# Optimization experiments

Measured on AMD Instinct MI355X. Metric: run time of the kernel, lower is better.

## Reference

```python
import jax, jax.numpy as jnp
import numpy as np

N, T, IN_DIM = 5000, 100, 32
FEAT, HID, OUT, HEADS = 64, 64, 8, 4
E = 160000
F_IN = FEAT + OUT  # GATCell input = concat(embedding, theta)


def setup_inputs() -> dict:
    key = jax.random.key(0)
    ks = jax.random.split(key, 16)
    s = 0.05
    d = {}
    d["x"] = jax.random.normal(ks[0], (N, T, IN_DIM), jnp.float32)
    d["edge_index"] = jax.random.randint(ks[1], (2, E), 0, N, dtype=jnp.int32)
    # LSTM params (PyTorch gate order: i, f, g, o)
    d["W_ih"] = jax.random.normal(ks[2], (IN_DIM, 4 * FEAT), jnp.float32) * s
    d["W_hh"] = jax.random.normal(ks[3], (FEAT, 4 * FEAT), jnp.float32) * s
    d["b_ih"] = jax.random.normal(ks[4], (4 * FEAT,), jnp.float32) * s
    d["b_hh"] = jax.random.normal(ks[5], (4 * FEAT,), jnp.float32) * s
    # TransformerConv params (lin_q/k/v with bias, lin_skip with bias; concat=False)
    d["Wq"] = jax.random.normal(ks[6], (F_IN, HEADS * HID), jnp.float32) * s
    d["bq"] = jax.random.normal(ks[7], (HEADS * HID,), jnp.float32) * s
    d["Wk"] = jax.random.normal(ks[8], (F_IN, HEADS * HID), jnp.float32) * s
    d["bk"] = jax.random.normal(ks[9], (HEADS * HID,), jnp.float32) * s
    d["Wv"] = jax.random.normal(ks[10], (F_IN, HEADS * HID), jnp.float32) * s
    d["bv"] = jax.random.normal(ks[11], (HEADS * HID,), jnp.float32) * s
    d["Wskip"] = jax.random.normal(ks[12], (F_IN, HID), jnp.float32) * s
    d["bskip"] = jax.random.normal(ks[13], (HID,), jnp.float32) * s
    # GATCell mlp (bias=False)
    d["Wmlp"] = jax.random.normal(ks[14], (HID, OUT), jnp.float32) * s
    return d


def _lstm(x, W_ih, W_hh, b_ih, b_hh):
    # x: [N, T, IN_DIM] -> embedding [T, N, FEAT]
    xs = jnp.transpose(x, (1, 0, 2))

    def step(carry, xt):
        h, c = carry
        gates = xt @ W_ih + h @ W_hh + (b_ih + b_hh)
        i, f, g, o = jnp.split(gates, 4, axis=-1)
        c = jax.nn.sigmoid(f) * c + jax.nn.sigmoid(i) * jnp.tanh(g)
        h = jax.nn.sigmoid(o) * jnp.tanh(c)
        return (h, c), h

    h0 = jnp.zeros((x.shape[0], FEAT), x.dtype)
    _, hs = jax.lax.scan(step, (h0, h0), xs)
    return hs


def _transformer_conv(h, edge_index, Wq, bq, Wk, bk, Wv, bv, Wskip, bskip):
    # h: [N, F_IN]; edge_index: [2, E] (row 0 = source j, row 1 = target i)
    n = h.shape[0]
    src, dst = edge_index[0], edge_index[1]
    q = (h @ Wq + bq).reshape(n, HEADS, HID)
    k = (h @ Wk + bk).reshape(n, HEADS, HID)
    v = (h @ Wv + bv).reshape(n, HEADS, HID)
    # per-edge attention logits [E, HEADS]
    alpha = jnp.einsum('ehd,ehd->eh', q[dst], k[src]) / jnp.sqrt(jnp.float32(HID))
    # segment softmax over incoming edges of each target node
    m = jax.ops.segment_max(alpha, dst, num_segments=n)
    m = jnp.where(jnp.isfinite(m), m, 0.0)
    ex = jnp.exp(alpha - m[dst])
    denom = jax.ops.segment_sum(ex, dst, num_segments=n)
    w = ex / jnp.maximum(denom[dst], 1e-16)
    agg = jax.ops.segment_sum(w[:, :, None] * v[src], dst, num_segments=n)  # [N,H,D]
    out = agg.mean(axis=1)  # concat=False -> average heads
    return out + h @ Wskip + bskip  # root skip connection


def reference(x, edge_index, W_ih, W_hh, b_ih, b_hh, Wq, bq, Wk, bk, Wv, bv,
              Wskip, bskip, Wmlp):
    emb = _lstm(x, W_ih, W_hh, b_ih, b_hh)  # [T, N, FEAT]
    n = x.shape[0]

    def gat_step(theta, emb_t):
        h_in = jnp.concatenate([emb_t, theta], axis=-1)  # [N, F_IN]
        hid = _transformer_conv(h_in, edge_index, Wq, bq, Wk, bk, Wv, bv,
                                Wskip, bskip)
        theta_new = jnp.tanh(hid) @ Wmlp
        return theta_new, theta_new

    theta0 = jnp.zeros((n, OUT), x.dtype)
    _, thetas = jax.lax.scan(gat_step, theta0, emb)  # [T, N, OUT]
    theta = jnp.transpose(thetas, (1, 0, 2))  # [N, T, OUT]

    alpha_beta = theta[:, :, :-3]
    a_b = jax.nn.sigmoid(theta[:, :, -3:-1])
    a = a_b[:, :, 0:1] * a_b[:, :, 1:]
    b = a_b[:, :, 0:1] - a
    c = jax.nn.softplus(theta[:, :, -1:])
    return jnp.concatenate([alpha_beta, a, b, c], axis=-1)
```

## Files before the change

### kernel.cpp

```cpp
#include <hip/hip_runtime.h>
#include <math.h>

#define NN 5000
#define TT 100
#define IND 32
#define FEATD 64
#define HIDD 64
#define OUTD 8
#define NHEADS 4
#define EE 160000
#define FIN 72
#define NHC 256
#define ATTN_B 2500
#define LSTM_B 625

typedef float floatx2 __attribute__((ext_vector_type(2)));

__device__ __forceinline__ float fsig(float x){ return 1.f/(1.f+__expf(-x)); }
__device__ __forceinline__ float ftanh(float x){ return 1.f - 2.f/(__expf(2.f*x)+1.f); }
__device__ __forceinline__ float fsoftplus(float x){ return (x>20.f)? x : log1pf(__expf(x)); }

__global__ __launch_bounds__(256) void count_edges(const int* __restrict__ dst,
                                                   int* __restrict__ cnt){
    int e = blockIdx.x*256 + threadIdx.x;
    if (e < EE) atomicAdd(&cnt[dst[e]], 1);
}

#define SCAN_N 5120
__global__ __launch_bounds__(1024) void scan_csr(const int* __restrict__ cnt,
                                                 int* __restrict__ row_ptr,
                                                 int* __restrict__ cursor){
    __shared__ int sa[SCAN_N];
    __shared__ int sb[SCAN_N];
    int tid = threadIdx.x;
    for (int i=tid;i<SCAN_N;i+=1024) sa[i] = (i<NN)?cnt[i]:0;
    __syncthreads();
    int *s=sa, *d=sb;
    for (int off=1; off<SCAN_N; off<<=1){
        for (int i=tid;i<SCAN_N;i+=1024){
            int v = s[i];
            if (i>=off) v += s[i-off];
            d[i] = v;
        }
        __syncthreads();
        int* t=s; s=d; d=t;
    }
    for (int i=tid;i<=NN;i+=1024){
        int excl = (i==0)?0:s[i-1];
        row_ptr[i] = excl;
        if (i<NN) cursor[i] = excl;
    }
}

__global__ __launch_bounds__(256) void fill_edges(const int* __restrict__ src,
                                                  const int* __restrict__ dst,
                                                  int* __restrict__ cursor,
                                                  int* __restrict__ col){
    int e = blockIdx.x*256 + threadIdx.x;
    if (e < EE){
        int dn = dst[e];
        int pos = atomicAdd(&cursor[dn], 1);
        col[pos] = src[e];
    }
}

#define LOADKV(e) (*reinterpret_cast<const uint2*>(kv + (size_t)col[(e)]*512 + lane*8))
__global__ __launch_bounds__(256) void lstm_attn_step(
    const float* __restrict__ x,
    const float* __restrict__ W_ih, const float* __restrict__ W_hh,
    const float* __restrict__ b_ih, const float* __restrict__ b_hh,
    float* __restrict__ h, float* __restrict__ c,
    const float* __restrict__ q,
    const unsigned char* __restrict__ kv,
    const float* __restrict__ sk,
    const int* __restrict__ row_ptr,
    const int* __restrict__ col,
    const float* __restrict__ Wmlp,
    float* __restrict__ theta,
    float* __restrict__ out,
    int t)
{
    __shared__ float mrg[2][5][64];
    __shared__ float xh[8][96];
    int tid = threadIdx.x;

    if (blockIdx.x < ATTN_B){
        if (t == 0) return;
        int wvid = tid >> 6;
        int lane = tid & 63;
        int ln   = wvid >> 1;
        int half = wvid & 1;
        int n = blockIdx.x*2 + ln;
        int e0 = row_ptr[n], e1 = row_ptr[n+1];
        float4 qv = *reinterpret_cast<const float4*>(q + n*NHC + lane*4);
        qv.x *= 0.125f; qv.y *= 0.125f; qv.z *= 0.125f; qv.w *= 0.125f;

        float denA=0.f, denB=0.f;
        float aA0=0.f, aA1=0.f, aA2=0.f, aA3=0.f;
        float aB0=0.f, aB1=0.f, aB2=0.f, aB3=0.f;

        const uint2 zv = {0u,0u};
        uint2 bA0=zv, bA1=zv, bB0=zv, bB1=zv;
        int base = e0 + half;
        if (base     < e1) bA0 = LOADKV(base);
        if (base + 2 < e1) bB0 = LOADKV(base+2);
        if (base + 4 < e1) bA1 = LOADKV(base+4);
        if (base + 6 < e1) bB1 = LOADKV(base+6);
        for (int e = base; e < e1; e += 4){
            uint2 uA = bA0; bA0 = bA1; bA1 = zv;
            uint2 uB = bB0; bB0 = bB1; bB1 = zv;
            if (e + 8  < e1) bA1 = LOADKV(e+8);
            if (e + 10 < e1) bB1 = LOADKV(e+10);

            floatx2 kA0 = __builtin_amdgcn_cvt_pk_f32_fp8(uA.x, false);
            floatx2 kA1 = __builtin_amdgcn_cvt_pk_f32_fp8(uA.x, true);
            floatx2 kB0 = __builtin_amdgcn_cvt_pk_f32_fp8(uB.x, false);
            floatx2 kB1 = __builtin_amdgcn_cvt_pk_f32_fp8(uB.x, true);
            float pA = qv.x*kA0[0] + qv.y*kA0[1] + qv.z*kA1[0] + qv.w*kA1[1];
            float pB = qv.x*kB0[0] + qv.y*kB0[1] + qv.z*kB1[0] + qv.w*kB1[1];
            pA += __shfl_xor(pA,1); pB += __shfl_xor(pB,1);
            pA += __shfl_xor(pA,2); pB += __shfl_xor(pB,2);
            pA += __shfl_xor(pA,4); pB += __shfl_xor(pB,4);
            pA += __shfl_xor(pA,8); pB += __shfl_xor(pB,8);

            float eA = __expf(pA);
            float eB = __expf((e + 2 < e1) ? pB : -INFINITY);
            floatx2 vA0 = __builtin_amdgcn_cvt_pk_f32_fp8(uA.y, false);
            floatx2 vA1 = __builtin_amdgcn_cvt_pk_f32_fp8(uA.y, true);
            floatx2 vB0 = __builtin_amdgcn_cvt_pk_f32_fp8(uB.y, false);
            floatx2 vB1 = __builtin_amdgcn_cvt_pk_f32_fp8(uB.y, true);
            denA += eA;
            aA0 = fmaf(eA, vA0[0], aA0);
            aA1 = fmaf(eA, vA0[1], aA1);
            aA2 = fmaf(eA, vA1[0], aA2);
            aA3 = fmaf(eA, vA1[1], aA3);
            denB += eB;
            aB0 = fmaf(eB, vB0[0], aB0);
            aB1 = fmaf(eB, vB0[1], aB1);
            aB2 = fmaf(eB, vB1[0], aB2);
            aB3 = fmaf(eB, vB1[1], aB3);
        }
        float denom = denA + denB;
        float ax = aA0 + aB0;
        float ay = aA1 + aB1;
        float az = aA2 + aB2;
        float aw = aA3 + aB3;

        if (half == 1){
            mrg[ln][0][lane]=denom;
            mrg[ln][1][lane]=ax; mrg[ln][2][lane]=ay;
            mrg[ln][3][lane]=az; mrg[ln][4][lane]=aw;
        }
        __syncthreads();
        if (half == 1) return;

        denom += mrg[ln][0][lane];
        ax += mrg[ln][1][lane];
        ay += mrg[ln][2][lane];
        az += mrg[ln][3][lane];
        aw += mrg[ln][4][lane];

        float inv = 1.f / fmaxf(denom, 1e-16f);
        ax *= inv; ay *= inv; az *= inv; aw *= inv;
        ax += __shfl_xor(ax,16); ax += __shfl_xor(ax,32);
        ay += __shfl_xor(ay,16); ay += __shfl_xor(ay,32);
        az += __shfl_xor(az,16); az += __shfl_xor(az,32);
        aw += __shfl_xor(aw,16); aw += __shfl_xor(aw,32);
        int d0 = (lane & 15) * 4;
        float4 skv = *reinterpret_cast<const float4*>(sk + n*64 + d0);
        float t0 = ftanh(0.25f*ax + skv.x);
        float t1 = ftanh(0.25f*ay + skv.y);
        float t2 = ftanh(0.25f*az + skv.z);
        float t3 = ftanh(0.25f*aw + skv.w);
        float p8[8];
        #pragma unroll
        for (int j=0;j<8;j++){
            p8[j] = fmaf(t0, Wmlp[(d0+0)*8+j],
                    fmaf(t1, Wmlp[(d0+1)*8+j],
                    fmaf(t2, Wmlp[(d0+2)*8+j],
                         t3* Wmlp[(d0+3)*8+j])));
        }
        #pragma unroll
        for (int j=0;j<8;j++){
            p8[j] += __shfl_xor(p8[j],1);
            p8[j] += __shfl_xor(p8[j],2);
            p8[j] += __shfl_xor(p8[j],4);
            p8[j] += __shfl_xor(p8[j],8);
        }
        if (lane == 0){
            float4 t0v = {p8[0],p8[1],p8[2],p8[3]};
            float4 t1v = {p8[4],p8[5],p8[6],p8[7]};
            *reinterpret_cast<float4*>(theta + n*8)     = t0v;
            *reinterpret_cast<float4*>(theta + n*8 + 4) = t1v;
            float ab0 = fsig(p8[5]);
            float ab1 = fsig(p8[6]);
            float a  = ab0*ab1;
            float bb = ab0 - a;
            float cc = fsoftplus(p8[7]);
            float4 o0 = {p8[0],p8[1],p8[2],p8[3]};
            float4 o1 = {p8[4],a,bb,cc};
            float* op = out + ((size_t)n*TT + (t-1))*8;
            *reinterpret_cast<float4*>(op)     = o0;
            *reinterpret_cast<float4*>(op + 4) = o1;
        }
    } else {
        if (t >= TT) return;
        int n0 = (blockIdx.x - ATTN_B) * 8;
        for (int i=tid; i<8*96; i+=256){
            int node = i/96, kk = i%96;
            int n = n0 + node;
            xh[node][kk] = (kk<32) ? x[(n*TT + t)*IND + kk] : h[n*64 + (kk-32)];
        }
        __syncthreads();

        int d  = tid & 63;
        int wv = tid >> 6;
        float acc[2][4];
        #pragma unroll
        for (int p=0;p<2;p++){
            #pragma unroll
            for (int g=0;g<4;g++) acc[p][g]=0.f;
        }
        #pragma unroll 8
        for (int kk=0; kk<32; kk++){
            const float* Wr = W_ih + kk*256;
            float w0=Wr[d], w1=Wr[d+64], w2=Wr[d+128], w3=Wr[d+192];
            float x0 = xh[wv][kk], x1 = xh[wv+4][kk];
            acc[0][0]=fmaf(x0,w0,acc[0][0]); acc[0][1]=fmaf(x0,w1,acc[0][1]);
            acc[0][2]=fmaf(x0,w2,acc[0][2]); acc[0][3]=fmaf(x0,w3,acc[0][3]);
            acc[1][0]=fmaf(x1,w0,acc[1][0]); acc[1][1]=fmaf(x1,w1,acc[1][1]);
            acc[1][2]=fmaf(x1,w2,acc[1][2]); acc[1][3]=fmaf(x1,w3,acc[1][3]);
        }
        #pragma unroll 8
        for (int kk=0; kk<64; kk++){
            const float* Wr = W_hh + kk*256;
            float w0=Wr[d], w1=Wr[d+64], w2=Wr[d+128], w3=Wr[d+192];
            float x0 = xh[wv][32+kk], x1 = xh[wv+4][32+kk];
            acc[0][0]=fmaf(x0,w0,acc[0][0]); acc[0][1]=fmaf(x0,w1,acc[0][1]);
            acc[0][2]=fmaf(x0,w2,acc[0][2]); acc[0][3]=fmaf(x0,w3,acc[0][3]);
            acc[1][0]=fmaf(x1,w0,acc[1][0]); acc[1][1]=fmaf(x1,w1,acc[1][1]);
            acc[1][2]=fmaf(x1,w2,acc[1][2]); acc[1][3]=fmaf(x1,w3,acc[1][3]);
        }
        float bi0 = b_ih[d]     + b_hh[d];
        float bi1 = b_ih[d+64]  + b_hh[d+64];
        float bi2 = b_ih[d+128] + b_hh[d+128];
        float bi3 = b_ih[d+192] + b_hh[d+192];
        #pragma unroll
        for (int p=0;p<2;p++){
            int n = n0 + wv + p*4;
            float gi = fsig (acc[p][0] + bi0);
            float gf = fsig (acc[p][1] + bi1);
            float gg = ftanh(acc[p][2] + bi2);
            float go = fsig (acc[p][3] + bi3);
            float cold = c[n*64 + d];
            float cnew = gf*cold + gi*gg;
            float hnew = go*ftanh(cnew);
            c[n*64 + d] = cnew;
            h[n*64 + d] = hnew;
        }
    }
}

__global__ __launch_bounds__(256) void qkv_step(
    const float* __restrict__ h, const float* __restrict__ theta,
    const float* __restrict__ Wq, const float* __restrict__ bq,
    const float* __restrict__ Wk, const float* __restrict__ bk,
    const float* __restrict__ Wv, const float* __restrict__ bv,
    const float* __restrict__ Wsk, const float* __restrict__ bsk,
    float* __restrict__ q, float* __restrict__ sk,
    unsigned char* __restrict__ kv)
{
    __shared__ float hin[8][72];
    int n0 = blockIdx.x * 8;
    int tid = threadIdx.x;
    for (int i=tid; i<8*72; i+=256){
        int node = i/72, kk = i%72;
        int n = n0 + node;
        hin[node][kk] = (kk<64) ? h[n*64+kk] : theta[n*8 + (kk-64)];
    }
    __syncthreads();

    if (tid < 208){
        int c4 = tid*4;
        const float* W; const float* b; int ncol; int cc; int kind;
        if (c4 < 256)      { W=Wq;  b=bq;  ncol=256; cc=c4;     kind=0; }
        else if (c4 < 512) { W=Wk;  b=bk;  ncol=256; cc=c4-256; kind=1; }
        else if (c4 < 768) { W=Wv;  b=bv;  ncol=256; cc=c4-512; kind=2; }
        else               { W=Wsk; b=bsk; ncol=64;  cc=c4-768; kind=3; }
        float acc2[8][4];
        #pragma unroll
        for (int nn=0;nn<8;nn++){
            #pragma unroll
            for (int j=0;j<4;j++) acc2[nn][j]=0.f;
        }
        #pragma unroll 4
        for (int kk=0; kk<FIN; kk++){
            float4 w = *reinterpret_cast<const float4*>(W + kk*ncol + cc);
            #pragma unroll
            for (int nn=0;nn<8;nn++){
                float xv = hin[nn][kk];
                acc2[nn][0]=fmaf(xv,w.x,acc2[nn][0]);
                acc2[nn][1]=fmaf(xv,w.y,acc2[nn][1]);
                acc2[nn][2]=fmaf(xv,w.z,acc2[nn][2]);
                acc2[nn][3]=fmaf(xv,w.w,acc2[nn][3]);
            }
        }
        float4 bb = *reinterpret_cast<const float4*>(b + cc);
        #pragma unroll
        for (int nn=0;nn<8;nn++){
            int n = n0 + nn;
            float o0=acc2[nn][0]+bb.x, o1=acc2[nn][1]+bb.y;
            float o2=acc2[nn][2]+bb.z, o3=acc2[nn][3]+bb.w;
            if (kind == 0){
                float4 o = {o0,o1,o2,o3};
                *reinterpret_cast<float4*>(q + n*NHC + cc) = o;
            } else if (kind == 3){
                float4 o = {o0,o1,o2,o3};
                *reinterpret_cast<float4*>(sk + n*64 + cc) = o;
            } else {
                int pk = __builtin_amdgcn_cvt_pk_fp8_f32(o0, o1, 0,  false);
                pk     = __builtin_amdgcn_cvt_pk_fp8_f32(o2, o3, pk, true);
                int off = n*512 + cc*2 + ((kind==2)?4:0);
                *reinterpret_cast<unsigned int*>(kv + off) = (unsigned int)pk;
            }
        }
    }
}

extern "C" void kernel_launch(void* const* d_in, const int* in_sizes, int n_in,
                              void* d_out, int out_size, void* d_ws, size_t ws_size,
                              hipStream_t stream) {
    const float* x     = (const float*)d_in[0];
    const int*   ei    = (const int*)  d_in[1];
    const float* W_ih  = (const float*)d_in[2];
    const float* W_hh  = (const float*)d_in[3];
    const float* b_ih  = (const float*)d_in[4];
    const float* b_hh  = (const float*)d_in[5];
    const float* Wq    = (const float*)d_in[6];
    const float* bq    = (const float*)d_in[7];
    const float* Wk    = (const float*)d_in[8];
    const float* bk    = (const float*)d_in[9];
    const float* Wv    = (const float*)d_in[10];
    const float* bv    = (const float*)d_in[11];
    const float* Wsk   = (const float*)d_in[12];
    const float* bsk   = (const float*)d_in[13];
    const float* Wmlp  = (const float*)d_in[14];
    float* out = (float*)d_out;

    float* f = (float*)d_ws;
    float* h     = f;
    float* c     = h + NN*64;
    float* theta = c + NN*64;
    float* q     = theta + NN*8;
    float* skb   = q + NN*NHC;
    unsigned char* kvb = (unsigned char*)(skb + NN*64);
    int* ip      = (int*)(kvb + (size_t)NN*512);
    int* row_ptr = ip;
    int* cnt     = row_ptr + (NN+1);
    int* cursor  = cnt + NN;
    int* colv    = cursor + NN;

    const int* src = ei;
    const int* dst = ei + EE;

    hipMemsetAsync(h, 0, (size_t)NN*(64+64+8)*sizeof(float), stream);
    hipMemsetAsync(cnt, 0, (size_t)NN*sizeof(int), stream);

    count_edges<<<(EE+255)/256, 256, 0, stream>>>(dst, cnt);
    scan_csr<<<1, 1024, 0, stream>>>(cnt, row_ptr, cursor);
    fill_edges<<<(EE+255)/256, 256, 0, stream>>>(src, dst, cursor, colv);

    for (int t=0; t<=TT; t++){
        lstm_attn_step<<<ATTN_B + LSTM_B, 256, 0, stream>>>(
            x, W_ih, W_hh, b_ih, b_hh, h, c,
            q, kvb, skb, row_ptr, colv, Wmlp, theta, out, t);
        if (t < TT)
            qkv_step<<<LSTM_B, 256, 0, stream>>>(h, theta,
                Wq,bq, Wk,bk, Wv,bv, Wsk,bsk, q, skb, kvb);
    }
}
```

Measured before the change: 4.762 ms.

## Co-schedule LSTM step with QKV projection using double-buffered hidden state

```diff
diff --git a/kernel.cpp b/kernel.cpp
--- a/kernel.cpp
+++ b/kernel.cpp
@@ -11,7 +11,7 @@
 #define EE 160000
 #define FIN 72
 #define NHC 256
-#define ATTN_B 2500
+#define QKV_B 625
 #define LSTM_B 625
 
 typedef float floatx2 __attribute__((ext_vector_type(2)));
@@ -65,11 +65,7 @@
 }
 
 #define LOADKV(e) (*reinterpret_cast<const uint2*>(kv + (size_t)col[(e)]*512 + lane*8))
-__global__ __launch_bounds__(256) void lstm_attn_step(
-    const float* __restrict__ x,
-    const float* __restrict__ W_ih, const float* __restrict__ W_hh,
-    const float* __restrict__ b_ih, const float* __restrict__ b_hh,
-    float* __restrict__ h, float* __restrict__ c,
+__global__ __launch_bounds__(256) void attn_step(
     const float* __restrict__ q,
     const unsigned char* __restrict__ kv,
     const float* __restrict__ sk,
@@ -78,138 +74,212 @@
     const float* __restrict__ Wmlp,
     float* __restrict__ theta,
     float* __restrict__ out,
-    int t)
+    int ts)
 {
     __shared__ float mrg[2][5][64];
-    __shared__ float xh[8][96];
     int tid = threadIdx.x;
-
-    if (blockIdx.x < ATTN_B){
-        if (t == 0) return;
-        int wvid = tid >> 6;
-        int lane = tid & 63;
-        int ln   = wvid >> 1;
-        int half = wvid & 1;
-        int n = blockIdx.x*2 + ln;
-        int e0 = row_ptr[n], e1 = row_ptr[n+1];
-        float4 qv = *reinterpret_cast<const float4*>(q + n*NHC + lane*4);
-        qv.x *= 0.125f; qv.y *= 0.125f; qv.z *= 0.125f; qv.w *= 0.125f;
-
-        float denA=0.f, denB=0.f;
-        float aA0=0.f, aA1=0.f, aA2=0.f, aA3=0.f;
-        float aB0=0.f, aB1=0.f, aB2=0.f, aB3=0.f;
-
-        const uint2 zv = {0u,0u};
-        uint2 bA0=zv, bA1=zv, bB0=zv, bB1=zv;
-        int base = e0 + half;
-        if (base     < e1) bA0 = LOADKV(base);
-        if (base + 2 < e1) bB0 = LOADKV(base+2);
-        if (base + 4 < e1) bA1 = LOADKV(base+4);
-        if (base + 6 < e1) bB1 = LOADKV(base+6);
-        for (int e = base; e < e1; e += 4){
-            uint2 uA = bA0; bA0 = bA1; bA1 = zv;
-            uint2 uB = bB0; bB0 = bB1; bB1 = zv;
-            if (e + 8  < e1) bA1 = LOADKV(e+8);
-            if (e + 10 < e1) bB1 = LOADKV(e+10);
-
-            floatx2 kA0 = __builtin_amdgcn_cvt_pk_f32_fp8(uA.x, false);
-            floatx2 kA1 = __builtin_amdgcn_cvt_pk_f32_fp8(uA.x, true);
-            floatx2 kB0 = __builtin_amdgcn_cvt_pk_f32_fp8(uB.x, false);
-            floatx2 kB1 = __builtin_amdgcn_cvt_pk_f32_fp8(uB.x, true);
-            float pA = qv.x*kA0[0] + qv.y*kA0[1] + qv.z*kA1[0] + qv.w*kA1[1];
-            float pB = qv.x*kB0[0] + qv.y*kB0[1] + qv.z*kB1[0] + qv.w*kB1[1];
-            pA += __shfl_xor(pA,1); pB += __shfl_xor(pB,1);
-            pA += __shfl_xor(pA,2); pB += __shfl_xor(pB,2);
-            pA += __shfl_xor(pA,4); pB += __shfl_xor(pB,4);
-            pA += __shfl_xor(pA,8); pB += __shfl_xor(pB,8);
-
-            float eA = __expf(pA);
-            float eB = __expf((e + 2 < e1) ? pB : -INFINITY);
-            floatx2 vA0 = __builtin_amdgcn_cvt_pk_f32_fp8(uA.y, false);
-            floatx2 vA1 = __builtin_amdgcn_cvt_pk_f32_fp8(uA.y, true);
-            floatx2 vB0 = __builtin_amdgcn_cvt_pk_f32_fp8(uB.y, false);
-            floatx2 vB1 = __builtin_amdgcn_cvt_pk_f32_fp8(uB.y, true);
-            denA += eA;
-            aA0 = fmaf(eA, vA0[0], aA0);
-            aA1 = fmaf(eA, vA0[1], aA1);
-            aA2 = fmaf(eA, vA1[0], aA2);
-            aA3 = fmaf(eA, vA1[1], aA3);
-            denB += eB;
-            aB0 = fmaf(eB, vB0[0], aB0);
-            aB1 = fmaf(eB, vB0[1], aB1);
-            aB2 = fmaf(eB, vB1[0], aB2);
-            aB3 = fmaf(eB, vB1[1], aB3);
-        }
-        float denom = denA + denB;
-        float ax = aA0 + aB0;
-        float ay = aA1 + aB1;
-        float az = aA2 + aB2;
-        float aw = aA3 + aB3;
-
-        if (half == 1){
-            mrg[ln][0][lane]=denom;
-            mrg[ln][1][lane]=ax; mrg[ln][2][lane]=ay;
-            mrg[ln][3][lane]=az; mrg[ln][4][lane]=aw;
+    int wvid = tid >> 6;
+    int lane = tid & 63;
+    int ln   = wvid >> 1;
+    int half = wvid & 1;
+    int n = blockIdx.x*2 + ln;
+    int e0 = row_ptr[n], e1 = row_ptr[n+1];
+    float4 qv = *reinterpret_cast<const float4*>(q + n*NHC + lane*4);
+    qv.x *= 0.125f; qv.y *= 0.125f; qv.z *= 0.125f; qv.w *= 0.125f;
+
+    float denA=0.f, denB=0.f;
+    float aA0=0.f, aA1=0.f, aA2=0.f, aA3=0.f;
+    float aB0=0.f, aB1=0.f, aB2=0.f, aB3=0.f;
+
+    const uint2 zv = {0u,0u};
+    uint2 bA0=zv, bA1=zv, bB0=zv, bB1=zv;
+    int base = e0 + half;
+    if (base     < e1) bA0 = LOADKV(base);
+    if (base + 2 < e1) bB0 = LOADKV(base+2);
+    if (base + 4 < e1) bA1 = LOADKV(base+4);
+    if (base + 6 < e1) bB1 = LOADKV(base+6);
+    for (int e = base; e < e1; e += 4){
+        uint2 uA = bA0; bA0 = bA1; bA1 = zv;
+        uint2 uB = bB0; bB0 = bB1; bB1 = zv;
+        if (e + 8  < e1) bA1 = LOADKV(e+8);
+        if (e + 10 < e1) bB1 = LOADKV(e+10);
+
+        floatx2 kA0 = __builtin_amdgcn_cvt_pk_f32_fp8(uA.x, false);
+        floatx2 kA1 = __builtin_amdgcn_cvt_pk_f32_fp8(uA.x, true);
+        floatx2 kB0 = __builtin_amdgcn_cvt_pk_f32_fp8(uB.x, false);
+        floatx2 kB1 = __builtin_amdgcn_cvt_pk_f32_fp8(uB.x, true);
+        float pA = qv.x*kA0[0] + qv.y*kA0[1] + qv.z*kA1[0] + qv.w*kA1[1];
+        float pB = qv.x*kB0[0] + qv.y*kB0[1] + qv.z*kB1[0] + qv.w*kB1[1];
+        pA += __shfl_xor(pA,1); pB += __shfl_xor(pB,1);
+        pA += __shfl_xor(pA,2); pB += __shfl_xor(pB,2);
+        pA += __shfl_xor(pA,4); pB += __shfl_xor(pB,4);
+        pA += __shfl_xor(pA,8); pB += __shfl_xor(pB,8);
+
+        float eA = __expf(pA);
+        float eB = __expf((e + 2 < e1) ? pB : -INFINITY);
+        floatx2 vA0 = __builtin_amdgcn_cvt_pk_f32_fp8(uA.y, false);
+        floatx2 vA1 = __builtin_amdgcn_cvt_pk_f32_fp8(uA.y, true);
+        floatx2 vB0 = __builtin_amdgcn_cvt_pk_f32_fp8(uB.y, false);
+        floatx2 vB1 = __builtin_amdgcn_cvt_pk_f32_fp8(uB.y, true);
+        denA += eA;
+        aA0 = fmaf(eA, vA0[0], aA0);
+        aA1 = fmaf(eA, vA0[1], aA1);
+        aA2 = fmaf(eA, vA1[0], aA2);
+        aA3 = fmaf(eA, vA1[1], aA3);
+        denB += eB;
+        aB0 = fmaf(eB, vB0[0], aB0);
+        aB1 = fmaf(eB, vB0[1], aB1);
+        aB2 = fmaf(eB, vB1[0], aB2);
+        aB3 = fmaf(eB, vB1[1], aB3);
+    }
+    float denom = denA + denB;
+    float ax = aA0 + aB0;
+    float ay = aA1 + aB1;
+    float az = aA2 + aB2;
+    float aw = aA3 + aB3;
+
+    if (half == 1){
+        mrg[ln][0][lane]=denom;
+        mrg[ln][1][lane]=ax; mrg[ln][2][lane]=ay;
+        mrg[ln][3][lane]=az; mrg[ln][4][lane]=aw;
+    }
+    __syncthreads();
+    if (half == 1) return;
+
+    denom += mrg[ln][0][lane];
+    ax += mrg[ln][1][lane];
+    ay += mrg[ln][2][lane];
+    az += mrg[ln][3][lane];
+    aw += mrg[ln][4][lane];
+
+    float inv = 1.f / fmaxf(denom, 1e-16f);
+    ax *= inv; ay *= inv; az *= inv; aw *= inv;
+    ax += __shfl_xor(ax,16); ax += __shfl_xor(ax,32);
+    ay += __shfl_xor(ay,16); ay += __shfl_xor(ay,32);
+    az += __shfl_xor(az,16); az += __shfl_xor(az,32);
+    aw += __shfl_xor(aw,16); aw += __shfl_xor(aw,32);
+    int d0 = (lane & 15) * 4;
+    float4 skv = *reinterpret_cast<const float4*>(sk + n*64 + d0);
+    float t0 = ftanh(0.25f*ax + skv.x);
+    float t1 = ftanh(0.25f*ay + skv.y);
+    float t2 = ftanh(0.25f*az + skv.z);
+    float t3 = ftanh(0.25f*aw + skv.w);
+    float p8[8];
+    #pragma unroll
+    for (int j=0;j<8;j++){
+        p8[j] = fmaf(t0, Wmlp[(d0+0)*8+j],
+                fmaf(t1, Wmlp[(d0+1)*8+j],
+                fmaf(t2, Wmlp[(d0+2)*8+j],
+                     t3* Wmlp[(d0+3)*8+j])));
+    }
+    #pragma unroll
+    for (int j=0;j<8;j++){
+        p8[j] += __shfl_xor(p8[j],1);
+        p8[j] += __shfl_xor(p8[j],2);
+        p8[j] += __shfl_xor(p8[j],4);
+        p8[j] += __shfl_xor(p8[j],8);
+    }
+    if (lane == 0){
+        float4 t0v = {p8[0],p8[1],p8[2],p8[3]};
+        float4 t1v = {p8[4],p8[5],p8[6],p8[7]};
+        *reinterpret_cast<float4*>(theta + n*8)     = t0v;
+        *reinterpret_cast<float4*>(theta + n*8 + 4) = t1v;
+        float ab0 = fsig(p8[5]);
+        float ab1 = fsig(p8[6]);
+        float a  = ab0*ab1;
+        float bb = ab0 - a;
+        float cc = fsoftplus(p8[7]);
+        float4 o0 = {p8[0],p8[1],p8[2],p8[3]};
+        float4 o1 = {p8[4],a,bb,cc};
+        float* op = out + ((size_t)n*TT + ts)*8;
+        *reinterpret_cast<float4*>(op)     = o0;
+        *reinterpret_cast<float4*>(op + 4) = o1;
+    }
+}
+
+__global__ __launch_bounds__(256) void qkv_lstm_step(
+    const float* __restrict__ x,
+    const float* __restrict__ W_ih, const float* __restrict__ W_hh,
+    const float* __restrict__ b_ih, const float* __restrict__ b_hh,
+    float* __restrict__ h0, float* __restrict__ h1,
+    float* __restrict__ c,
+    const float* __restrict__ theta,
+    const float* __restrict__ Wq, const float* __restrict__ bq,
+    const float* __restrict__ Wk, const float* __restrict__ bk,
+    const float* __restrict__ Wv, const float* __restrict__ bv,
+    const float* __restrict__ Wsk, const float* __restrict__ bsk,
+    float* __restrict__ q, float* __restrict__ sk,
+    unsigned char* __restrict__ kv, int t)
+{
+    int tid = threadIdx.x;
+    if (blockIdx.x < QKV_B){
+        if (t < 0) return;
+        __shared__ float hin[8][72];
+        const float* hread = (t & 1) ? h1 : h0;
+        int n0 = blockIdx.x * 8;
+        for (int i=tid; i<8*72; i+=256){
+            int node = i/72, kk = i%72;
+            int n = n0 + node;
+            hin[node][kk] = (kk<64) ? hread[n*64+kk] : theta[n*8 + (kk-64)];
         }
         __syncthreads();
-        if (half == 1) return;
-
-        denom += mrg[ln][0][lane];
-        ax += mrg[ln][1][lane];
-        ay += mrg[ln][2][lane];
-        az += mrg[ln][3][lane];
-        aw += mrg[ln][4][lane];
-
-        float inv = 1.f / fmaxf(denom, 1e-16f);
-        ax *= inv; ay *= inv; az *= inv; aw *= inv;
-        ax += __shfl_xor(ax,16); ax += __shfl_xor(ax,32);
-        ay += __shfl_xor(ay,16); ay += __shfl_xor(ay,32);
-        az += __shfl_xor(az,16); az += __shfl_xor(az,32);
-        aw += __shfl_xor(aw,16); aw += __shfl_xor(aw,32);
-        int d0 = (lane & 15) * 4;
-        float4 skv = *reinterpret_cast<const float4*>(sk + n*64 + d0);
-        float t0 = ftanh(0.25f*ax + skv.x);
-        float t1 = ftanh(0.25f*ay + skv.y);
-        float t2 = ftanh(0.25f*az + skv.z);
-        float t3 = ftanh(0.25f*aw + skv.w);
-        float p8[8];
-        #pragma unroll
-        for (int j=0;j<8;j++){
-            p8[j] = fmaf(t0, Wmlp[(d0+0)*8+j],
-                    fmaf(t1, Wmlp[(d0+1)*8+j],
-                    fmaf(t2, Wmlp[(d0+2)*8+j],
-                         t3* Wmlp[(d0+3)*8+j])));
-        }
-        #pragma unroll
-        for (int j=0;j<8;j++){
-            p8[j] += __shfl_xor(p8[j],1);
-            p8[j] += __shfl_xor(p8[j],2);
-            p8[j] += __shfl_xor(p8[j],4);
-            p8[j] += __shfl_xor(p8[j],8);
-        }
-        if (lane == 0){
-            float4 t0v = {p8[0],p8[1],p8[2],p8[3]};
-            float4 t1v = {p8[4],p8[5],p8[6],p8[7]};
-            *reinterpret_cast<float4*>(theta + n*8)     = t0v;
-            *reinterpret_cast<float4*>(theta + n*8 + 4) = t1v;
-            float ab0 = fsig(p8[5]);
-            float ab1 = fsig(p8[6]);
-            float a  = ab0*ab1;
-            float bb = ab0 - a;
-            float cc = fsoftplus(p8[7]);
-            float4 o0 = {p8[0],p8[1],p8[2],p8[3]};
-            float4 o1 = {p8[4],a,bb,cc};
-            float* op = out + ((size_t)n*TT + (t-1))*8;
-            *reinterpret_cast<float4*>(op)     = o0;
-            *reinterpret_cast<float4*>(op + 4) = o1;
+
+        if (tid < 208){
+            int c4 = tid*4;
+            const float* W; const float* b; int ncol; int cc; int kind;
+            if (c4 < 256)      { W=Wq;  b=bq;  ncol=256; cc=c4;     kind=0; }
+            else if (c4 < 512) { W=Wk;  b=bk;  ncol=256; cc=c4-256; kind=1; }
+            else if (c4 < 768) { W=Wv;  b=bv;  ncol=256; cc=c4-512; kind=2; }
+            else               { W=Wsk; b=bsk; ncol=64;  cc=c4-768; kind=3; }
+            float acc2[8][4];
+            #pragma unroll
+            for (int nn=0;nn<8;nn++){
+                #pragma unroll
+                for (int j=0;j<4;j++) acc2[nn][j]=0.f;
+            }
+            #pragma unroll 4
+            for (int kk=0; kk<FIN; kk++){
+                float4 w = *reinterpret_cast<const float4*>(W + kk*ncol + cc);
+                #pragma unroll
+                for (int nn=0;nn<8;nn++){
+                    float xv = hin[nn][kk];
+                    acc2[nn][0]=fmaf(xv,w.x,acc2[nn][0]);
+                    acc2[nn][1]=fmaf(xv,w.y,acc2[nn][1]);
+                    acc2[nn][2]=fmaf(xv,w.z,acc2[nn][2]);
+                    acc2[nn][3]=fmaf(xv,w.w,acc2[nn][3]);
+                }
+            }
+            float4 bb = *reinterpret_cast<const float4*>(b + cc);
+            #pragma unroll
+            for (int nn=0;nn<8;nn++){
+                int n = n0 + nn;
+                float o0=acc2[nn][0]+bb.x, o1=acc2[nn][1]+bb.y;
+                float o2=acc2[nn][2]+bb.z, o3=acc2[nn][3]+bb.w;
+                if (kind == 0){
+                    float4 o = {o0,o1,o2,o3};
+                    *reinterpret_cast<float4*>(q + n*NHC + cc) = o;
+                } else if (kind == 3){
+                    float4 o = {o0,o1,o2,o3};
+                    *reinterpret_cast<float4*>(sk + n*64 + cc) = o;
+                } else {
+                    int pk = __builtin_amdgcn_cvt_pk_fp8_f32(o0, o1, 0,  false);
+                    pk     = __builtin_amdgcn_cvt_pk_fp8_f32(o2, o3, pk, true);
+                    int off = n*512 + cc*2 + ((kind==2)?4:0);
+                    *reinterpret_cast<unsigned int*>(kv + off) = (unsigned int)pk;
+                }
+            }
         }
     } else {
-        if (t >= TT) return;
-        int n0 = (blockIdx.x - ATTN_B) * 8;
+        int s = t + 1;
+        if (s >= TT) return;
+        __shared__ float xh[8][96];
+        const float* hread = (s & 1) ? h0 : h1;
+        float*       hwrit = (s & 1) ? h1 : h0;
+        int n0 = (blockIdx.x - QKV_B) * 8;
         for (int i=tid; i<8*96; i+=256){
             int node = i/96, kk = i%96;
             int n = n0 + node;
-            xh[node][kk] = (kk<32) ? x[(n*TT + t)*IND + kk] : h[n*64 + (kk-32)];
+            xh[node][kk] = (kk<32) ? x[(n*TT + s)*IND + kk] : hread[n*64 + (kk-32)];
         }
         __syncthreads();
 
@@ -256,73 +326,7 @@
             float cnew = gf*cold + gi*gg;
             float hnew = go*ftanh(cnew);
             c[n*64 + d] = cnew;
-            h[n*64 + d] = hnew;
-        }
-    }
-}
-
-__global__ __launch_bounds__(256) void qkv_step(
-    const float* __restrict__ h, const float* __restrict__ theta,
-    const float* __restrict__ Wq, const float* __restrict__ bq,
-    const float* __restrict__ Wk, const float* __restrict__ bk,
-    const float* __restrict__ Wv, const float* __restrict__ bv,
-    const float* __restrict__ Wsk, const float* __restrict__ bsk,
-    float* __restrict__ q, float* __restrict__ sk,
-    unsigned char* __restrict__ kv)
-{
-    __shared__ float hin[8][72];
-    int n0 = blockIdx.x * 8;
-    int tid = threadIdx.x;
-    for (int i=tid; i<8*72; i+=256){
-        int node = i/72, kk = i%72;
-        int n = n0 + node;
-        hin[node][kk] = (kk<64) ? h[n*64+kk] : theta[n*8 + (kk-64)];
-    }
-    __syncthreads();
-
-    if (tid < 208){
-        int c4 = tid*4;
-        const float* W; const float* b; int ncol; int cc; int kind;
-        if (c4 < 256)      { W=Wq;  b=bq;  ncol=256; cc=c4;     kind=0; }
-        else if (c4 < 512) { W=Wk;  b=bk;  ncol=256; cc=c4-256; kind=1; }
-        else if (c4 < 768) { W=Wv;  b=bv;  ncol=256; cc=c4-512; kind=2; }
-        else               { W=Wsk; b=bsk; ncol=64;  cc=c4-768; kind=3; }
-        float acc2[8][4];
-        #pragma unroll
-        for (int nn=0;nn<8;nn++){
-            #pragma unroll
-            for (int j=0;j<4;j++) acc2[nn][j]=0.f;
-        }
-        #pragma unroll 4
-        for (int kk=0; kk<FIN; kk++){
-            float4 w = *reinterpret_cast<const float4*>(W + kk*ncol + cc);
-            #pragma unroll
-            for (int nn=0;nn<8;nn++){
-                float xv = hin[nn][kk];
-                acc2[nn][0]=fmaf(xv,w.x,acc2[nn][0]);
-                acc2[nn][1]=fmaf(xv,w.y,acc2[nn][1]);
-                acc2[nn][2]=fmaf(xv,w.z,acc2[nn][2]);
-                acc2[nn][3]=fmaf(xv,w.w,acc2[nn][3]);
-            }
-        }
-        float4 bb = *reinterpret_cast<const float4*>(b + cc);
-        #pragma unroll
-        for (int nn=0;nn<8;nn++){
-            int n = n0 + nn;
-            float o0=acc2[nn][0]+bb.x, o1=acc2[nn][1]+bb.y;
-            float o2=acc2[nn][2]+bb.z, o3=acc2[nn][3]+bb.w;
-            if (kind == 0){
-                float4 o = {o0,o1,o2,o3};
-                *reinterpret_cast<float4*>(q + n*NHC + cc) = o;
-            } else if (kind == 3){
-                float4 o = {o0,o1,o2,o3};
-                *reinterpret_cast<float4*>(sk + n*64 + cc) = o;
-            } else {
-                int pk = __builtin_amdgcn_cvt_pk_fp8_f32(o0, o1, 0,  false);
-                pk     = __builtin_amdgcn_cvt_pk_fp8_f32(o2, o3, pk, true);
-                int off = n*512 + cc*2 + ((kind==2)?4:0);
-                *reinterpret_cast<unsigned int*>(kv + off) = (unsigned int)pk;
-            }
+            hwrit[n*64 + d] = hnew;
         }
     }
 }
@@ -348,8 +352,9 @@
     float* out = (float*)d_out;
 
     float* f = (float*)d_ws;
-    float* h     = f;
-    float* c     = h + NN*64;
+    float* h0    = f;
+    float* h1    = h0 + NN*64;
+    float* c     = h1 + NN*64;
     float* theta = c + NN*64;
     float* q     = theta + NN*8;
     float* skb   = q + NN*NHC;
@@ -363,19 +368,25 @@
     const int* src = ei;
     const int* dst = ei + EE;
 
-    hipMemsetAsync(h, 0, (size_t)NN*(64+64+8)*sizeof(float), stream);
+    hipMemsetAsync(h0, 0, (size_t)NN*(64+64+64+8)*sizeof(float), stream);
     hipMemsetAsync(cnt, 0, (size_t)NN*sizeof(int), stream);
 
     count_edges<<<(EE+255)/256, 256, 0, stream>>>(dst, cnt);
     scan_csr<<<1, 1024, 0, stream>>>(cnt, row_ptr, cursor);
     fill_edges<<<(EE+255)/256, 256, 0, stream>>>(src, dst, cursor, colv);
 
-    for (int t=0; t<=TT; t++){
-        lstm_attn_step<<<ATTN_B + LSTM_B, 256, 0, stream>>>(
-            x, W_ih, W_hh, b_ih, b_hh, h, c,
-            q, kvb, skb, row_ptr, colv, Wmlp, theta, out, t);
-        if (t < TT)
-            qkv_step<<<LSTM_B, 256, 0, stream>>>(h, theta,
-                Wq,bq, Wk,bk, Wv,bv, Wsk,bsk, q, skb, kvb);
-    }
-}
+    qkv_lstm_step<<<QKV_B + LSTM_B, 256, 0, stream>>>(
+        x, W_ih, W_hh, b_ih, b_hh, h0, h1, c, theta,
+        Wq,bq, Wk,bk, Wv,bv, Wsk,bsk, q, skb, kvb, -1);
+
+    for (int t=0; t<TT; t++){
+        if (t >= 1)
+            attn_step<<<NN/2, 256, 0, stream>>>(q, kvb, skb, row_ptr, colv,
+                                                Wmlp, theta, out, t-1);
+        qkv_lstm_step<<<QKV_B + LSTM_B, 256, 0, stream>>>(
+            x, W_ih, W_hh, b_ih, b_hh, h0, h1, c, theta,
+            Wq,bq, Wk,bk, Wv,bv, Wsk,bsk, q, skb, kvb, t);
+    }
+    attn_step<<<NN/2, 256, 0, stream>>>(q, kvb, skb, row_ptr, colv,
+                                        Wmlp, theta, out, TT-1);
+}
```

New measurement: 5.073 ms. 6.5% more time.
